# Kernel tuning notes

Measured on AMD Instinct MI355X. Metric: run time of the kernel, lower is better.

## Reference

```python
import jax, jax.numpy as jnp
import numpy as np

DIM = 2048
N_HEADS = 32
N_KV_HEADS = 8
HEAD_DIM = 64
BATCH = 2
SEQ = 2048
N_REP = N_HEADS // N_KV_HEADS
SCALE = HEAD_DIM ** -0.5
ROPE_BASE = 10000.0


def setup_inputs() -> dict:
    key = jax.random.key(0)
    ks = jax.random.split(key, 5)
    x = jax.random.normal(ks[0], (BATCH, SEQ, DIM), dtype=jnp.float32)
    # weights stored as (in, out) so projection is x @ W
    Wq = jax.random.normal(ks[1], (DIM, N_HEADS * HEAD_DIM), dtype=jnp.float32) * (DIM ** -0.5)
    Wk = jax.random.normal(ks[2], (DIM, N_KV_HEADS * HEAD_DIM), dtype=jnp.float32) * (DIM ** -0.5)
    Wv = jax.random.normal(ks[3], (DIM, N_KV_HEADS * HEAD_DIM), dtype=jnp.float32) * (DIM ** -0.5)
    Wo = jax.random.normal(ks[4], (N_HEADS * HEAD_DIM, DIM), dtype=jnp.float32) * ((N_HEADS * HEAD_DIM) ** -0.5)
    # RoPE tables (seq, head_dim)
    inv_freq = 1.0 / (ROPE_BASE ** (jnp.arange(0, HEAD_DIM, 2, dtype=jnp.float32) / HEAD_DIM))
    t = jnp.arange(SEQ, dtype=jnp.float32)
    freqs = jnp.outer(t, inv_freq)                      # (S, D/2)
    emb = jnp.concatenate([freqs, freqs], axis=-1)      # (S, D)
    cos = jnp.cos(emb)
    sin = jnp.sin(emb)
    # additive causal mask (1,1,S,S)
    neg = jnp.finfo(jnp.float32).min
    causal = jnp.tril(jnp.ones((SEQ, SEQ), dtype=bool))
    attention_mask = jnp.where(causal, 0.0, neg)[None, None, :, :].astype(jnp.float32)
    return {"x": x, "Wq": Wq, "Wk": Wk, "Wv": Wv, "Wo": Wo,
            "cos": cos, "sin": sin, "attention_mask": attention_mask}


def _rotate_half(u):
    h = u.shape[-1] // 2
    return jnp.concatenate([-u[..., h:], u[..., :h]], axis=-1)


def reference(x, Wq, Wk, Wv, Wo, cos, sin, attention_mask):
    b, s, _ = x.shape
    q = (x @ Wq).reshape(b, s, N_HEADS, HEAD_DIM)
    k = (x @ Wk).reshape(b, s, N_KV_HEADS, HEAD_DIM)
    v = (x @ Wv).reshape(b, s, N_KV_HEADS, HEAD_DIM)
    # RoPE, broadcast over head dim (unsqueeze_dim=2)
    c = cos[None, :, None, :]
    sn = sin[None, :, None, :]
    q = q * c + _rotate_half(q) * sn
    k = k * c + _rotate_half(k) * sn
    # repeat KV heads for GQA: (b,s,kvh,d) -> (b,s,h,d)
    k = jnp.repeat(k, N_REP, axis=2)
    v = jnp.repeat(v, N_REP, axis=2)
    # (b,h,s,d)
    q = q.transpose(0, 2, 1, 3)
    k = k.transpose(0, 2, 1, 3)
    v = v.transpose(0, 2, 1, 3)
    scores = jnp.einsum("bhqd,bhkd->bhqk", q, k) * SCALE + attention_mask
    attn = jax.nn.softmax(scores.astype(jnp.float32), axis=-1).astype(q.dtype)
    out = jnp.einsum("bhqk,bhkd->bhqd", attn, v)
    out = out.transpose(0, 2, 1, 3).reshape(b, s, N_HEADS * HEAD_DIM)
    return out @ Wo
```

## Files before the change

### kernel.cpp

```cpp
#include <hip/hip_runtime.h>
#include <hip/hip_bf16.h>

typedef unsigned short u16;
typedef unsigned int   u32;
typedef __bf16 bf16_t;
typedef bf16_t bf16x8 __attribute__((ext_vector_type(8)));
typedef u16    u16x8  __attribute__((ext_vector_type(8)));
typedef float  f32x4  __attribute__((ext_vector_type(4)));

#define DIM  2048
#define SEQ  2048
#define BATCH 2
#define NH   32
#define NKVH 8
#define HD   64
#define KVDIM (NKVH*HD)
#define NQKV (DIM + 2*KVDIM)
#define SCALE 0.125f

__device__ __forceinline__ float b2f(u16 u) {
  union { u32 i; float f; } v; v.i = ((u32)u) << 16; return v.f;
}
__device__ __forceinline__ u16 f2b(float f) {
  union { float f; u32 i; } v; v.f = f;
  u32 x = v.i;
  return (u16)((x + 0x7fffu + ((x >> 16) & 1u)) >> 16);
}
__device__ __forceinline__ u32 pkbf2(float a, float b) {
  __hip_bfloat162 h = __float22bfloat162_rn(float2{a, b});
  union { __hip_bfloat162 h; u32 u; } v; v.h = h; return v.u;
}
__device__ __forceinline__ int probe_bf16(const u32* probe) { return probe[0] != 0u; }
__device__ __forceinline__ float ext_ld(const void* p, long idx, int mode_bf16) {
  return mode_bf16 ? b2f(((const u16*)p)[idx]) : ((const float*)p)[idx];
}
__device__ __forceinline__ void gload_lds16(const u16* g, u16* l) {
  __builtin_amdgcn_global_load_lds((const __attribute__((address_space(1))) void*)g,
                                   (__attribute__((address_space(3))) void*)l, 16, 0, 0);
}

__global__ void cast_x(const void* __restrict__ in, u16* __restrict__ out,
                       const u32* __restrict__ probe) {
  int mode = probe_bf16(probe);
  long base = ((long)blockIdx.x * 256 + threadIdx.x) * 8;
  if (mode) {
    *(uint4*)&out[base] = *(const uint4*)((const u16*)in + base);
  } else {
    float4 f0 = *(const float4*)((const float*)in + base);
    float4 f1 = *(const float4*)((const float*)in + base + 4);
    u16x8 t;
    t[0] = f2b(f0.x); t[1] = f2b(f0.y); t[2] = f2b(f0.z); t[3] = f2b(f0.w);
    t[4] = f2b(f1.x); t[5] = f2b(f1.y); t[6] = f2b(f1.z); t[7] = f2b(f1.w);
    *(u16x8*)&out[base] = t;
  }
}

__global__ void transpose_qkv(const void* __restrict__ Wq, const void* __restrict__ Wk,
                              const void* __restrict__ Wv, u16* __restrict__ out,
                              const u32* __restrict__ probe) {
  int mode = probe_bf16(probe);
  __shared__ u16 t[32][33];
  int xt = blockIdx.x;
  const void* in; int C, c0, obase;
  if (xt < 64)      { in = Wq; C = DIM;   c0 = xt * 32;        obase = 0; }
  else if (xt < 80) { in = Wk; C = KVDIM; c0 = (xt - 64) * 32; obase = DIM; }
  else              { in = Wv; C = KVDIM; c0 = (xt - 80) * 32; obase = DIM + KVDIM; }
  int r0 = blockIdx.y * 32;
  int tx = threadIdx.x, ty = threadIdx.y;
#pragma unroll
  for (int i = 0; i < 32; i += 8)
    t[ty + i][tx] = mode ? ((const u16*)in)[(long)(r0 + ty + i) * C + c0 + tx]
                         : f2b(((const float*)in)[(long)(r0 + ty + i) * C + c0 + tx]);
  __syncthreads();
#pragma unroll
  for (int i = 0; i < 32; i += 8)
    out[(long)(obase + c0 + ty + i) * DIM + r0 + tx] = t[tx][ty + i];
}

__global__ void transpose_w(const void* __restrict__ in, u16* __restrict__ out,
                            int R, int C, const u32* __restrict__ probe) {
  int mode = probe_bf16(probe);
  __shared__ u16 t[32][33];
  int c0 = blockIdx.x * 32, r0 = blockIdx.y * 32;
  int tx = threadIdx.x, ty = threadIdx.y;
#pragma unroll
  for (int i = 0; i < 32; i += 8)
    t[ty + i][tx] = mode ? ((const u16*)in)[(long)(r0 + ty + i) * C + c0 + tx]
                         : f2b(((const float*)in)[(long)(r0 + ty + i) * C + c0 + tx]);
  __syncthreads();
#pragma unroll
  for (int i = 0; i < 32; i += 8)
    out[(long)(c0 + ty + i) * R + r0 + tx] = t[tx][ty + i];
}

__global__ void rope_both(u16* __restrict__ Qb, u16* __restrict__ Kb,
                          const void* __restrict__ cosb, const void* __restrict__ sinb,
                          const u32* __restrict__ probe) {
  int mode = probe_bf16(probe);
  long gid = (long)blockIdx.x * 256 + threadIdx.x;
  const long NQp = (long)BATCH * SEQ * NH * 32;
  u16* base_p; int n_heads; long t; float osc;
  if (gid < NQp) { base_p = Qb; n_heads = NH; t = gid; osc = SCALE; }
  else           { base_p = Kb; n_heads = NKVH; t = gid - NQp; osc = 1.0f; }
  int pair = t & 31;
  long t2 = t >> 5;
  int h = (int)(t2 % n_heads);
  long row = t2 / n_heads;
  int s = (int)(row & (SEQ - 1));
  long base = row * (n_heads * HD) + h * HD + pair;
  float q0 = b2f(base_p[base]), q1 = b2f(base_p[base + 32]);
  float c0 = ext_ld(cosb, (long)s * HD + pair, mode);
  float c1 = ext_ld(cosb, (long)s * HD + pair + 32, mode);
  float s0 = ext_ld(sinb, (long)s * HD + pair, mode);
  float s1 = ext_ld(sinb, (long)s * HD + pair + 32, mode);
  base_p[base]      = f2b((q0 * c0 - q1 * s0) * osc);
  base_p[base + 32] = f2b((q1 * c1 + q0 * s1) * osc);
}


__launch_bounds__(256)
__global__ void gemm_qkv(const void* __restrict__ A, const u16* __restrict__ Bt,
                         u16* __restrict__ Qb, u16* __restrict__ Kb, u16* __restrict__ Vt,
                         int a_half, const u32* __restrict__ probe) {
  int mode = a_half || probe_bf16(probe);
  __shared__ __align__(16) u16 As[128 * 32];
  __shared__ __align__(16) u16 Bs[128 * 32];
  int tid = threadIdx.x, lane = tid & 63, wv = tid >> 6;
  int l16 = lane & 15, q = lane >> 4;
  int bm0 = blockIdx.y * 128, bn0 = blockIdx.x * 128;
  int mbase = (wv & 1) * 64, nbase = (wv >> 1) * 64;
  int c0 = tid, c1 = tid + 256;
  int r0 = c0 >> 2, s0 = (c0 & 3) ^ ((r0 >> 1) & 3);
  int r1 = c1 >> 2, s1 = (c1 & 3) ^ ((r1 >> 1) & 3);
  const int K = DIM;
  long aoff0 = (long)(bm0 + r0) * K + s0 * 8;
  long aoff1 = (long)(bm0 + r1) * K + s1 * 8;
  long boff0 = (long)(bn0 + r0) * K + s0 * 8;
  long boff1 = (long)(bn0 + r1) * K + s1 * 8;
  int rsw = (q ^ ((l16 >> 1) & 3)) * 8;
  f32x4 acc[4][4] = {};
  for (int k0 = 0; k0 < K; k0 += 32) {
    __syncthreads();
    if (mode) {
      gload_lds16((const u16*)A + aoff0 + k0, &As[wv * 512]);
      gload_lds16((const u16*)A + aoff1 + k0, &As[2048 + wv * 512]);
    } else {
      const float* Af = (const float*)A;
      float4 f0 = *(const float4*)(Af + aoff0 + k0);
      float4 f1 = *(const float4*)(Af + aoff0 + k0 + 4);
      u16x8 t;
      t[0] = f2b(f0.x); t[1] = f2b(f0.y); t[2] = f2b(f0.z); t[3] = f2b(f0.w);
      t[4] = f2b(f1.x); t[5] = f2b(f1.y); t[6] = f2b(f1.z); t[7] = f2b(f1.w);
      *(u16x8*)&As[c0 * 8] = t;
      float4 g0 = *(const float4*)(Af + aoff1 + k0);
      float4 g1 = *(const float4*)(Af + aoff1 + k0 + 4);
      u16x8 u;
      u[0] = f2b(g0.x); u[1] = f2b(g0.y); u[2] = f2b(g0.z); u[3] = f2b(g0.w);
      u[4] = f2b(g1.x); u[5] = f2b(g1.y); u[6] = f2b(g1.z); u[7] = f2b(g1.w);
      *(u16x8*)&As[c1 * 8] = u;
    }
    gload_lds16(Bt + boff0 + k0, &Bs[wv * 512]);
    gload_lds16(Bt + boff1 + k0, &Bs[2048 + wv * 512]);
    __syncthreads();
    bf16x8 af[4], bfr[4];
#pragma unroll
    for (int mi = 0; mi < 4; mi++)
      af[mi] = *(const bf16x8*)&As[(mbase + mi * 16 + l16) * 32 + rsw];
#pragma unroll
    for (int ni = 0; ni < 4; ni++)
      bfr[ni] = *(const bf16x8*)&Bs[(nbase + ni * 16 + l16) * 32 + rsw];
#pragma unroll
    for (int mi = 0; mi < 4; mi++)
#pragma unroll
      for (int ni = 0; ni < 4; ni++)
        acc[mi][ni] = __builtin_amdgcn_mfma_f32_16x16x32_bf16(
            af[mi], bfr[ni], acc[mi][ni], 0, 0, 0);
  }
  if (bn0 < DIM + KVDIM) {
    u16* Cb; int ldc, ncol0;
    if (bn0 < DIM) { Cb = Qb; ldc = DIM; ncol0 = bn0; }
    else           { Cb = Kb; ldc = KVDIM; ncol0 = bn0 - DIM; }
#pragma unroll
    for (int mi = 0; mi < 4; mi++)
#pragma unroll
      for (int ni = 0; ni < 4; ni++)
#pragma unroll
        for (int r = 0; r < 4; r++) {
          int m = bm0 + mbase + mi * 16 + q * 4 + r;
          int n = ncol0 + nbase + ni * 16 + l16;
          Cb[(long)m * ldc + n] = f2b(acc[mi][ni][r]);
        }
  } else {
    int vcol0 = bn0 - DIM - KVDIM;
#pragma unroll
    for (int mi = 0; mi < 4; mi++)
#pragma unroll
      for (int ni = 0; ni < 4; ni++) {
        int vcol = vcol0 + nbase + ni * 16 + l16;
        int kvh2 = vcol >> 6, d = vcol & 63;
        int m = bm0 + mbase + mi * 16 + q * 4;
        int bb = m >> 11, s = m & (SEQ - 1);
        uint2 w;
        w.x = pkbf2(acc[mi][ni][0], acc[mi][ni][1]);
        w.y = pkbf2(acc[mi][ni][2], acc[mi][ni][3]);
        *(uint2*)&Vt[((long)(bb * NKVH + kvh2) * HD + d) * SEQ + s] = w;
      }
  }
}

__launch_bounds__(256)
__global__ void gemm_ao(const u16* __restrict__ A, const u16* __restrict__ Bt,
                        void* __restrict__ C, const u32* __restrict__ probe) {
  int mode = probe_bf16(probe);
  __shared__ __align__(16) u16 As[128 * 32];
  __shared__ __align__(16) u16 Bs[128 * 32];
  int tid = threadIdx.x, lane = tid & 63, wv = tid >> 6;
  int l16 = lane & 15, q = lane >> 4;
  int bm0 = blockIdx.y * 128, bn0 = blockIdx.x * 128;
  int mbase = (wv & 1) * 64, nbase = (wv >> 1) * 64;
  int c0 = tid, c1 = tid + 256;
  int r0 = c0 >> 2, s0 = (c0 & 3) ^ ((r0 >> 1) & 3);
  int r1 = c1 >> 2, s1 = (c1 & 3) ^ ((r1 >> 1) & 3);
  const int K = DIM;
  long aoff0 = (long)(bm0 + r0) * K + s0 * 8;
  long aoff1 = (long)(bm0 + r1) * K + s1 * 8;
  long boff0 = (long)(bn0 + r0) * K + s0 * 8;
  long boff1 = (long)(bn0 + r1) * K + s1 * 8;
  int rsw = (q ^ ((l16 >> 1) & 3)) * 8;
  f32x4 acc[4][4] = {};
  for (int k0 = 0; k0 < K; k0 += 32) {
    __syncthreads();
    gload_lds16(A + aoff0 + k0, &As[wv * 512]);
    gload_lds16(A + aoff1 + k0, &As[2048 + wv * 512]);
    gload_lds16(Bt + boff0 + k0, &Bs[wv * 512]);
    gload_lds16(Bt + boff1 + k0, &Bs[2048 + wv * 512]);
    __syncthreads();
    bf16x8 af[4], bfr[4];
#pragma unroll
    for (int mi = 0; mi < 4; mi++)
      af[mi] = *(const bf16x8*)&As[(mbase + mi * 16 + l16) * 32 + rsw];
#pragma unroll
    for (int ni = 0; ni < 4; ni++)
      bfr[ni] = *(const bf16x8*)&Bs[(nbase + ni * 16 + l16) * 32 + rsw];
#pragma unroll
    for (int mi = 0; mi < 4; mi++)
#pragma unroll
      for (int ni = 0; ni < 4; ni++)
        acc[mi][ni] = __builtin_amdgcn_mfma_f32_16x16x32_bf16(
            af[mi], bfr[ni], acc[mi][ni], 0, 0, 0);
  }
#pragma unroll
  for (int mi = 0; mi < 4; mi++)
#pragma unroll
    for (int ni = 0; ni < 4; ni++)
#pragma unroll
      for (int r = 0; r < 4; r++) {
        int m = bm0 + mbase + mi * 16 + q * 4 + r;
        int n = bn0 + nbase + ni * 16 + l16;
        if (mode) ((u16*)C)[(long)m * DIM + n] = f2b(acc[mi][ni][r]);
        else      ((float*)C)[(long)m * DIM + n] = acc[mi][ni][r];
      }
}

__launch_bounds__(256, 4)
__global__ void attn_kernel(const u16* __restrict__ Q, const u16* __restrict__ K,
                            const u16* __restrict__ Vt, u16* __restrict__ AO) {
  __shared__ __align__(16) u16 Ks[64 * 64];
  __shared__ __align__(16) u16 Vs[64 * 64];
  __shared__ __align__(16) u16 Ps[4][16 * 64];
  int tid = threadIdx.x, lane = tid & 63, wv = tid >> 6;
  int l16 = lane & 15, q = lane >> 4;
  int i = blockIdx.x;
  int bh = blockIdx.y;
  int b = bh >> 5, h = bh & 31, kvh = h >> 2;
  const u16* Kp = K + (long)b * SEQ * KVDIM + kvh * HD;
  const u16* Vp = Vt + (long)(b * NKVH + kvh) * HD * SEQ;

  int cA = tid, cB = tid + 256;
  int rA = cA >> 3, bA = (cA & 7) ^ (rA & 7);
  int rB = cB >> 3, bB = (cB & 7) ^ (rB & 7);
  const u16* kSrcA = Kp + (long)rA * KVDIM + bA * 8;
  const u16* kSrcB = Kp + (long)rB * KVDIM + bB * 8;
  const u16* vSrcA = Vp + (long)rA * SEQ + bA * 8;
  const u16* vSrcB = Vp + (long)rB * SEQ + bB * 8;
  u16* kDstA = &Ks[(wv * 64 + lane) * 8];
  u16* kDstB = &Ks[(256 + wv * 64 + lane) * 8];
  u16* vDstA = &Vs[(wv * 64 + lane) * 8];
  u16* vDstB = &Vs[(256 + wv * 64 + lane) * 8];

  int e = l16 & 7;
  int off0 = (q ^ e) * 8;
  int off1 = ((4 + q) ^ e) * 8;

  bf16x8 ones;
#pragma unroll
  for (int j = 0; j < 8; j++) ones[j] = (bf16_t)1.0f;

#pragma unroll
  for (int ph = 0; ph < 2; ph++) {
    int t = ph ? (31 - i) : i;
    int qbase = t * 64 + wv * 16;
    const u16* Qp = Q + (long)(b * SEQ + qbase) * DIM + h * HD;
    bf16x8 aq0 = *(const bf16x8*)&Qp[l16 * DIM + q * 8];
    bf16x8 aq1 = *(const bf16x8*)&Qp[l16 * DIM + 32 + q * 8];
    f32x4 o_acc[4] = {};
    f32x4 l_acc = {};
    int qrow = qbase + l16;

    for (int kt = 0; kt <= t; kt++) {
      long kk = (long)kt * 64;
      __syncthreads();
      gload_lds16(kSrcA + kk * KVDIM, kDstA);
      gload_lds16(kSrcB + kk * KVDIM, kDstB);
      gload_lds16(vSrcA + kk, vDstA);
      gload_lds16(vSrcB + kk, vDstB);
      __syncthreads();

      f32x4 sc[4];
#pragma unroll
      for (int ni = 0; ni < 4; ni++) {
        bf16x8 bk0 = *(const bf16x8*)&Ks[(ni * 16 + l16) * 64 + off0];
        bf16x8 bk1 = *(const bf16x8*)&Ks[(ni * 16 + l16) * 64 + off1];
        f32x4 z = {};
        z = __builtin_amdgcn_mfma_f32_16x16x32_bf16(bk0, aq0, z, 0, 0, 0);
        z = __builtin_amdgcn_mfma_f32_16x16x32_bf16(bk1, aq1, z, 0, 0, 0);
        sc[ni] = z;
      }
      if (kt == t) {
#pragma unroll
        for (int ni = 0; ni < 4; ni++)
#pragma unroll
          for (int r = 0; r < 4; r++) {
            int kv = (int)kk + ni * 16 + q * 4 + r;
            float p = __expf(sc[ni][r]);
            sc[ni][r] = (kv <= qrow) ? p : 0.f;
          }
      } else {
#pragma unroll
        for (int ni = 0; ni < 4; ni++)
#pragma unroll
          for (int r = 0; r < 4; r++) sc[ni][r] = __expf(sc[ni][r]);
      }
#pragma unroll
      for (int ni = 0; ni < 4; ni++) {
        uint2 w;
        w.x = pkbf2(sc[ni][0], sc[ni][1]);
        w.y = pkbf2(sc[ni][2], sc[ni][3]);
        int pblk = (2 * ni + (q >> 1)) ^ e;
        *(uint2*)&Ps[wv][l16 * 64 + pblk * 8 + (q & 1) * 4] = w;
      }
      bf16x8 ap0 = *(const bf16x8*)&Ps[wv][l16 * 64 + off0];
      bf16x8 ap1 = *(const bf16x8*)&Ps[wv][l16 * 64 + off1];
      l_acc = __builtin_amdgcn_mfma_f32_16x16x32_bf16(ap0, ones, l_acc, 0, 0, 0);
      l_acc = __builtin_amdgcn_mfma_f32_16x16x32_bf16(ap1, ones, l_acc, 0, 0, 0);
#pragma unroll
      for (int di = 0; di < 4; di++) {
        bf16x8 bv0 = *(const bf16x8*)&Vs[(di * 16 + l16) * 64 + off0];
        bf16x8 bv1 = *(const bf16x8*)&Vs[(di * 16 + l16) * 64 + off1];
        o_acc[di] = __builtin_amdgcn_mfma_f32_16x16x32_bf16(ap0, bv0, o_acc[di], 0, 0, 0);
        o_acc[di] = __builtin_amdgcn_mfma_f32_16x16x32_bf16(ap1, bv1, o_acc[di], 0, 0, 0);
      }
    }
    long obase = (long)(b * SEQ + qbase + q * 4) * DIM + h * HD;
#pragma unroll
    for (int r = 0; r < 4; r++) {
      float inv = 1.0f / l_acc[r];
#pragma unroll
      for (int di = 0; di < 4; di++)
        AO[obase + (long)r * DIM + di * 16 + l16] = f2b(o_acc[di][r] * inv);
    }
  }
}

extern "C" void kernel_launch(void* const* d_in, const int* in_sizes, int n_in,
                              void* d_out, int out_size, void* d_ws, size_t ws_size,
                              hipStream_t stream) {
  const void* x    = d_in[0];
  const void* Wq   = d_in[1];
  const void* Wk   = d_in[2];
  const void* Wv   = d_in[3];
  const void* Wo   = d_in[4];
  const void* cosb = d_in[5];
  const void* sinb = d_in[6];
  const u32*  probe = (const u32*)d_in[7];

  u16* WqkvT = (u16*)d_ws;
  u16* WoT = WqkvT + (size_t)NQKV * DIM;
  u16* Qb  = WoT + (size_t)DIM * DIM;
  u16* Kb  = Qb  + (size_t)BATCH * SEQ * DIM;
  u16* Vt  = Kb  + (size_t)BATCH * SEQ * KVDIM;
  u16* xb  = Vt  + (size_t)BATCH * NKVH * HD * SEQ;
  u16* AO  = Qb;

  size_t need_xb = ((size_t)(xb - WqkvT) + (size_t)BATCH * SEQ * DIM) * sizeof(u16);
  int use_xb = ws_size >= need_xb;

  dim3 blk32(32, 8);
  transpose_qkv<<<dim3(96, 64), blk32, 0, stream>>>(Wq, Wk, Wv, WqkvT, probe);
  transpose_w<<<dim3(DIM / 32, DIM / 32), blk32, 0, stream>>>(Wo, WoT, DIM, DIM, probe);

  int M = BATCH * SEQ;
  if (use_xb) {
    cast_x<<<(M * DIM) / (256 * 8), 256, 0, stream>>>(x, xb, probe);
    gemm_qkv<<<dim3(NQKV / 128, M / 128), 256, 0, stream>>>(xb, WqkvT, Qb, Kb, Vt, 1, probe);
  } else {
    gemm_qkv<<<dim3(NQKV / 128, M / 128), 256, 0, stream>>>(x, WqkvT, Qb, Kb, Vt, 0, probe);
  }

  long rope_slots = (long)M * NH * 32 + (long)M * NKVH * 32;
  rope_both<<<(int)(rope_slots / 256), 256, 0, stream>>>(Qb, Kb, cosb, sinb, probe);

  attn_kernel<<<dim3(16, BATCH * NH), 256, 0, stream>>>(Qb, Kb, Vt, AO);

  gemm_ao<<<dim3(DIM / 128, M / 128), 256, 0, stream>>>(AO, WoT, d_out, probe);
}
```

Before: 327.2 us.

## Double-buffer attention KV tiles, remap GEMM tiles per XCD, vectorize epilogue stores

Gives the attention kernel a double-buffered K/V LDS tile so the next tile's global-to-LDS load is issued while the current one is computed, leaving one barrier per iteration instead of two. Both GEMMs remap workgroup IDs so tiles sharing B columns land on the same XCD, for better L2 reuse. The GEMM MFMA operands are swapped so each lane holds four consecutive output columns, which lets the epilogue use packed 8- or 16-byte stores instead of scalar stores. cast_x skips its copy when the input is already bf16, and gemm_qkv reads x directly in that case. The cost is twice the K/V LDS in attention, which may lower occupancy.

```diff
diff --git a/kernel.cpp b/kernel.cpp
--- a/kernel.cpp
+++ b/kernel.cpp
@@ -39,20 +39,20 @@
                                    (__attribute__((address_space(3))) void*)l, 16, 0, 0);
 }
 
+struct SwapT   { static constexpr bool value = true;  };
+struct NoSwapT { static constexpr bool value = false; };
+
 __global__ void cast_x(const void* __restrict__ in, u16* __restrict__ out,
                        const u32* __restrict__ probe) {
   int mode = probe_bf16(probe);
+  if (mode) return;
   long base = ((long)blockIdx.x * 256 + threadIdx.x) * 8;
-  if (mode) {
-    *(uint4*)&out[base] = *(const uint4*)((const u16*)in + base);
-  } else {
-    float4 f0 = *(const float4*)((const float*)in + base);
-    float4 f1 = *(const float4*)((const float*)in + base + 4);
-    u16x8 t;
-    t[0] = f2b(f0.x); t[1] = f2b(f0.y); t[2] = f2b(f0.z); t[3] = f2b(f0.w);
-    t[4] = f2b(f1.x); t[5] = f2b(f1.y); t[6] = f2b(f1.z); t[7] = f2b(f1.w);
-    *(u16x8*)&out[base] = t;
-  }
+  float4 f0 = *(const float4*)((const float*)in + base);
+  float4 f1 = *(const float4*)((const float*)in + base + 4);
+  u16x8 t;
+  t[0] = f2b(f0.x); t[1] = f2b(f0.y); t[2] = f2b(f0.z); t[3] = f2b(f0.w);
+  t[4] = f2b(f1.x); t[5] = f2b(f1.y); t[6] = f2b(f1.z); t[7] = f2b(f1.w);
+  *(u16x8*)&out[base] = t;
 }
 
 __global__ void transpose_qkv(const void* __restrict__ Wq, const void* __restrict__ Wk,
@@ -119,15 +119,22 @@
 
 
 __launch_bounds__(256)
-__global__ void gemm_qkv(const void* __restrict__ A, const u16* __restrict__ Bt,
+__global__ void gemm_qkv(const void* __restrict__ x, const u16* __restrict__ xb,
+                         int use_xb, const u16* __restrict__ Bt,
                          u16* __restrict__ Qb, u16* __restrict__ Kb, u16* __restrict__ Vt,
-                         int a_half, const u32* __restrict__ probe) {
-  int mode = a_half || probe_bf16(probe);
+                         const u32* __restrict__ probe) {
+  int pmode = probe_bf16(probe);
+  int mode = (use_xb || pmode) ? 1 : 0;
+  const u16* A16 = pmode ? (const u16*)x : xb;
+  const float* Af = (const float*)x;
   __shared__ __align__(16) u16 As[128 * 32];
   __shared__ __align__(16) u16 Bs[128 * 32];
   int tid = threadIdx.x, lane = tid & 63, wv = tid >> 6;
   int l16 = lane & 15, q = lane >> 4;
-  int bm0 = blockIdx.y * 128, bn0 = blockIdx.x * 128;
+  int wg = blockIdx.y * 24 + blockIdx.x;
+  int xcd = wg & 7, tch = wg >> 3;
+  int bm0 = (tch / 3) * 128;
+  int bn0 = (xcd * 3 + tch % 3) * 128;
   int mbase = (wv & 1) * 64, nbase = (wv >> 1) * 64;
   int c0 = tid, c1 = tid + 256;
   int r0 = c0 >> 2, s0 = (c0 & 3) ^ ((r0 >> 1) & 3);
@@ -139,58 +146,70 @@
   long boff1 = (long)(bn0 + r1) * K + s1 * 8;
   int rsw = (q ^ ((l16 >> 1) & 3)) * 8;
   f32x4 acc[4][4] = {};
-  for (int k0 = 0; k0 < K; k0 += 32) {
-    __syncthreads();
-    if (mode) {
-      gload_lds16((const u16*)A + aoff0 + k0, &As[wv * 512]);
-      gload_lds16((const u16*)A + aoff1 + k0, &As[2048 + wv * 512]);
-    } else {
-      const float* Af = (const float*)A;
-      float4 f0 = *(const float4*)(Af + aoff0 + k0);
-      float4 f1 = *(const float4*)(Af + aoff0 + k0 + 4);
-      u16x8 t;
-      t[0] = f2b(f0.x); t[1] = f2b(f0.y); t[2] = f2b(f0.z); t[3] = f2b(f0.w);
-      t[4] = f2b(f1.x); t[5] = f2b(f1.y); t[6] = f2b(f1.z); t[7] = f2b(f1.w);
-      *(u16x8*)&As[c0 * 8] = t;
-      float4 g0 = *(const float4*)(Af + aoff1 + k0);
-      float4 g1 = *(const float4*)(Af + aoff1 + k0 + 4);
-      u16x8 u;
-      u[0] = f2b(g0.x); u[1] = f2b(g0.y); u[2] = f2b(g0.z); u[3] = f2b(g0.w);
-      u[4] = f2b(g1.x); u[5] = f2b(g1.y); u[6] = f2b(g1.z); u[7] = f2b(g1.w);
-      *(u16x8*)&As[c1 * 8] = u;
+
+  auto kloop = [&](auto tag) {
+    constexpr bool SWAP = decltype(tag)::value;
+    for (int k0 = 0; k0 < K; k0 += 32) {
+      __syncthreads();
+      if (mode) {
+        gload_lds16(A16 + aoff0 + k0, &As[wv * 512]);
+        gload_lds16(A16 + aoff1 + k0, &As[2048 + wv * 512]);
+      } else {
+        float4 f0 = *(const float4*)(Af + aoff0 + k0);
+        float4 f1 = *(const float4*)(Af + aoff0 + k0 + 4);
+        u16x8 t;
+        t[0] = f2b(f0.x); t[1] = f2b(f0.y); t[2] = f2b(f0.z); t[3] = f2b(f0.w);
+        t[4] = f2b(f1.x); t[5] = f2b(f1.y); t[6] = f2b(f1.z); t[7] = f2b(f1.w);
+        *(u16x8*)&As[c0 * 8] = t;
+        float4 g0 = *(const float4*)(Af + aoff1 + k0);
+        float4 g1 = *(const float4*)(Af + aoff1 + k0 + 4);
+        u16x8 u;
+        u[0] = f2b(g0.x); u[1] = f2b(g0.y); u[2] = f2b(g0.z); u[3] = f2b(g0.w);
+        u[4] = f2b(g1.x); u[5] = f2b(g1.y); u[6] = f2b(g1.z); u[7] = f2b(g1.w);
+        *(u16x8*)&As[c1 * 8] = u;
+      }
+      gload_lds16(Bt + boff0 + k0, &Bs[wv * 512]);
+      gload_lds16(Bt + boff1 + k0, &Bs[2048 + wv * 512]);
+      __syncthreads();
+      bf16x8 af[4], bfr[4];
+#pragma unroll
+      for (int mi = 0; mi < 4; mi++)
+        af[mi] = *(const bf16x8*)&As[(mbase + mi * 16 + l16) * 32 + rsw];
+#pragma unroll
+      for (int ni = 0; ni < 4; ni++)
+        bfr[ni] = *(const bf16x8*)&Bs[(nbase + ni * 16 + l16) * 32 + rsw];
+#pragma unroll
+      for (int mi = 0; mi < 4; mi++)
+#pragma unroll
+        for (int ni = 0; ni < 4; ni++) {
+          if constexpr (SWAP)
+            acc[mi][ni] = __builtin_amdgcn_mfma_f32_16x16x32_bf16(
+                bfr[ni], af[mi], acc[mi][ni], 0, 0, 0);
+          else
+            acc[mi][ni] = __builtin_amdgcn_mfma_f32_16x16x32_bf16(
+                af[mi], bfr[ni], acc[mi][ni], 0, 0, 0);
+        }
     }
-    gload_lds16(Bt + boff0 + k0, &Bs[wv * 512]);
-    gload_lds16(Bt + boff1 + k0, &Bs[2048 + wv * 512]);
-    __syncthreads();
-    bf16x8 af[4], bfr[4];
-#pragma unroll
-    for (int mi = 0; mi < 4; mi++)
-      af[mi] = *(const bf16x8*)&As[(mbase + mi * 16 + l16) * 32 + rsw];
-#pragma unroll
-    for (int ni = 0; ni < 4; ni++)
-      bfr[ni] = *(const bf16x8*)&Bs[(nbase + ni * 16 + l16) * 32 + rsw];
-#pragma unroll
-    for (int mi = 0; mi < 4; mi++)
-#pragma unroll
-      for (int ni = 0; ni < 4; ni++)
-        acc[mi][ni] = __builtin_amdgcn_mfma_f32_16x16x32_bf16(
-            af[mi], bfr[ni], acc[mi][ni], 0, 0, 0);
-  }
+  };
+
   if (bn0 < DIM + KVDIM) {
+    kloop(SwapT{});
     u16* Cb; int ldc, ncol0;
     if (bn0 < DIM) { Cb = Qb; ldc = DIM; ncol0 = bn0; }
     else           { Cb = Kb; ldc = KVDIM; ncol0 = bn0 - DIM; }
 #pragma unroll
     for (int mi = 0; mi < 4; mi++)
 #pragma unroll
-      for (int ni = 0; ni < 4; ni++)
-#pragma unroll
-        for (int r = 0; r < 4; r++) {
-          int m = bm0 + mbase + mi * 16 + q * 4 + r;
-          int n = ncol0 + nbase + ni * 16 + l16;
-          Cb[(long)m * ldc + n] = f2b(acc[mi][ni][r]);
-        }
+      for (int ni = 0; ni < 4; ni++) {
+        int m = bm0 + mbase + mi * 16 + l16;
+        int n0 = ncol0 + nbase + ni * 16 + q * 4;
+        uint2 w;
+        w.x = pkbf2(acc[mi][ni][0], acc[mi][ni][1]);
+        w.y = pkbf2(acc[mi][ni][2], acc[mi][ni][3]);
+        *(uint2*)&Cb[(long)m * ldc + n0] = w;
+      }
   } else {
+    kloop(NoSwapT{});
     int vcol0 = bn0 - DIM - KVDIM;
 #pragma unroll
     for (int mi = 0; mi < 4; mi++)
@@ -216,7 +235,10 @@
   __shared__ __align__(16) u16 Bs[128 * 32];
   int tid = threadIdx.x, lane = tid & 63, wv = tid >> 6;
   int l16 = lane & 15, q = lane >> 4;
-  int bm0 = blockIdx.y * 128, bn0 = blockIdx.x * 128;
+  int wg = blockIdx.y * 16 + blockIdx.x;
+  int xcd = wg & 7, tch = wg >> 3;
+  int bm0 = (tch / 2) * 128;
+  int bn0 = (xcd * 2 + tch % 2) * 128;
   int mbase = (wv & 1) * 64, nbase = (wv >> 1) * 64;
   int c0 = tid, c1 = tid + 256;
   int r0 = c0 >> 2, s0 = (c0 & 3) ^ ((r0 >> 1) & 3);
@@ -247,26 +269,33 @@
 #pragma unroll
       for (int ni = 0; ni < 4; ni++)
         acc[mi][ni] = __builtin_amdgcn_mfma_f32_16x16x32_bf16(
-            af[mi], bfr[ni], acc[mi][ni], 0, 0, 0);
+            bfr[ni], af[mi], acc[mi][ni], 0, 0, 0);
   }
 #pragma unroll
   for (int mi = 0; mi < 4; mi++)
 #pragma unroll
-    for (int ni = 0; ni < 4; ni++)
-#pragma unroll
-      for (int r = 0; r < 4; r++) {
-        int m = bm0 + mbase + mi * 16 + q * 4 + r;
-        int n = bn0 + nbase + ni * 16 + l16;
-        if (mode) ((u16*)C)[(long)m * DIM + n] = f2b(acc[mi][ni][r]);
-        else      ((float*)C)[(long)m * DIM + n] = acc[mi][ni][r];
-      }
+    for (int ni = 0; ni < 4; ni++) {
+      int m = bm0 + mbase + mi * 16 + l16;
+      int n0 = bn0 + nbase + ni * 16 + q * 4;
+      if (mode) {
+        uint2 w;
+        w.x = pkbf2(acc[mi][ni][0], acc[mi][ni][1]);
+        w.y = pkbf2(acc[mi][ni][2], acc[mi][ni][3]);
+        *(uint2*)&((u16*)C)[(long)m * DIM + n0] = w;
+      } else {
+        float4 f;
+        f.x = acc[mi][ni][0]; f.y = acc[mi][ni][1];
+        f.z = acc[mi][ni][2]; f.w = acc[mi][ni][3];
+        *(float4*)&((float*)C)[(long)m * DIM + n0] = f;
+      }
+    }
 }
 
 __launch_bounds__(256, 4)
 __global__ void attn_kernel(const u16* __restrict__ Q, const u16* __restrict__ K,
                             const u16* __restrict__ Vt, u16* __restrict__ AO) {
-  __shared__ __align__(16) u16 Ks[64 * 64];
-  __shared__ __align__(16) u16 Vs[64 * 64];
+  __shared__ __align__(16) u16 Ks[2 * 64 * 64];
+  __shared__ __align__(16) u16 Vs[2 * 64 * 64];
   __shared__ __align__(16) u16 Ps[4][16 * 64];
   int tid = threadIdx.x, lane = tid & 63, wv = tid >> 6;
   int l16 = lane & 15, q = lane >> 4;
@@ -307,20 +336,32 @@
     f32x4 l_acc = {};
     int qrow = qbase + l16;
 
+    __syncthreads();
+    gload_lds16(kSrcA, kDstA);
+    gload_lds16(kSrcB, kDstB);
+    gload_lds16(vSrcA, vDstA);
+    gload_lds16(vSrcB, vDstB);
+    int curo = 0;
+
     for (int kt = 0; kt <= t; kt++) {
+      __syncthreads();
+      if (kt < t) {
+        long kk2 = (long)(kt + 1) * 64;
+        int nxt = curo ^ 4096;
+        gload_lds16(kSrcA + kk2 * KVDIM, kDstA + nxt);
+        gload_lds16(kSrcB + kk2 * KVDIM, kDstB + nxt);
+        gload_lds16(vSrcA + kk2, vDstA + nxt);
+        gload_lds16(vSrcB + kk2, vDstB + nxt);
+      }
+      const u16* Ksb = &Ks[curo];
+      const u16* Vsb = &Vs[curo];
       long kk = (long)kt * 64;
-      __syncthreads();
-      gload_lds16(kSrcA + kk * KVDIM, kDstA);
-      gload_lds16(kSrcB + kk * KVDIM, kDstB);
-      gload_lds16(vSrcA + kk, vDstA);
-      gload_lds16(vSrcB + kk, vDstB);
-      __syncthreads();
 
       f32x4 sc[4];
 #pragma unroll
       for (int ni = 0; ni < 4; ni++) {
-        bf16x8 bk0 = *(const bf16x8*)&Ks[(ni * 16 + l16) * 64 + off0];
-        bf16x8 bk1 = *(const bf16x8*)&Ks[(ni * 16 + l16) * 64 + off1];
+        bf16x8 bk0 = *(const bf16x8*)&Ksb[(ni * 16 + l16) * 64 + off0];
+        bf16x8 bk1 = *(const bf16x8*)&Ksb[(ni * 16 + l16) * 64 + off1];
         f32x4 z = {};
         z = __builtin_amdgcn_mfma_f32_16x16x32_bf16(bk0, aq0, z, 0, 0, 0);
         z = __builtin_amdgcn_mfma_f32_16x16x32_bf16(bk1, aq1, z, 0, 0, 0);
@@ -355,11 +396,12 @@
       l_acc = __builtin_amdgcn_mfma_f32_16x16x32_bf16(ap1, ones, l_acc, 0, 0, 0);
 #pragma unroll
       for (int di = 0; di < 4; di++) {
-        bf16x8 bv0 = *(const bf16x8*)&Vs[(di * 16 + l16) * 64 + off0];
-        bf16x8 bv1 = *(const bf16x8*)&Vs[(di * 16 + l16) * 64 + off1];
+        bf16x8 bv0 = *(const bf16x8*)&Vsb[(di * 16 + l16) * 64 + off0];
+        bf16x8 bv1 = *(const bf16x8*)&Vsb[(di * 16 + l16) * 64 + off1];
         o_acc[di] = __builtin_amdgcn_mfma_f32_16x16x32_bf16(ap0, bv0, o_acc[di], 0, 0, 0);
         o_acc[di] = __builtin_amdgcn_mfma_f32_16x16x32_bf16(ap1, bv1, o_acc[di], 0, 0, 0);
       }
+      curo ^= 4096;
     }
     long obase = (long)(b * SEQ + qbase + q * 4) * DIM + h * HD;
 #pragma unroll
@@ -402,9 +444,9 @@
   int M = BATCH * SEQ;
   if (use_xb) {
     cast_x<<<(M * DIM) / (256 * 8), 256, 0, stream>>>(x, xb, probe);
-    gemm_qkv<<<dim3(NQKV / 128, M / 128), 256, 0, stream>>>(xb, WqkvT, Qb, Kb, Vt, 1, probe);
+    gemm_qkv<<<dim3(NQKV / 128, M / 128), 256, 0, stream>>>(x, xb, 1, WqkvT, Qb, Kb, Vt, probe);
   } else {
-    gemm_qkv<<<dim3(NQKV / 128, M / 128), 256, 0, stream>>>(x, WqkvT, Qb, Kb, Vt, 0, probe);
+    gemm_qkv<<<dim3(NQKV / 128, M / 128), 256, 0, stream>>>(x, nullptr, 0, WqkvT, Qb, Kb, Vt, probe);
   }
 
   long rope_slots = (long)M * NH * 32 + (long)M * NKVH * 32;
```

Result: no change. 331.1 us (+1.2%).
